# Kernel tuning notes

Hardware: AMD Instinct MI355X
Metric: run time of the kernel (lower is better)

## Reference

```python
import jax, jax.numpy as jnp
import numpy as np

LAGS = 2
LATENT = 64          # latent_size; number of tiny per-dim MLPs
HID = 64             # hidden_dim of each MLP2
SLOPE = 0.2          # LeakyReLU negative slope
IN_DIM = LAGS * LATENT + 1  # 129: flattened lags + current value of dim i


def setup_inputs() -> dict:
    key = jax.random.key(0)
    k0, k1, k2, k3, k4 = jax.random.split(key, 5)
    B, LEN = 32, 512
    x = jax.random.normal(k0, (B, LEN + LAGS, LATENT), jnp.float32)
    # Stacked per-latent MLP2 params (num_layers=1):
    #   Linear(IN_DIM -> HID) + LeakyReLU(0.2) + Linear(HID -> 1)
    s1 = float(1.0 / np.sqrt(IN_DIM))
    s2 = float(1.0 / np.sqrt(HID))
    W1 = jax.random.uniform(k1, (LATENT, HID, IN_DIM), jnp.float32, -s1, s1)
    b1 = jax.random.uniform(k2, (LATENT, HID), jnp.float32, -s1, s1)
    W2 = jax.random.uniform(k3, (LATENT, HID), jnp.float32, -s2, s2)
    b2 = jax.random.uniform(k4, (LATENT,), jnp.float32, -s2, s2)
    return {"x": x, "W1": W1, "b1": b1, "W2": W2, "b2": b2}


def reference(x, W1, b1, W2, b2):
    B, T, xd = x.shape
    length = T - LAGS
    N = B * length
    # torch unfold(dim=1, size=LAGS+1, step=1).transpose(2,3) -> [B, length, LAGS+1, xd]
    idx = jnp.arange(length)[:, None] + jnp.arange(LAGS + 1)[None, :]
    win = x[:, idx]                                   # [B, length, LAGS+1, xd]
    lagsx = win[:, :, :-1].reshape(N, LAGS * xd)      # [N, LAGS*xd]
    xt = win[:, :, -1].reshape(N, xd)                 # [N, xd] current values per latent dim
    # gs[i] input = concat(lagsx, xt[:, i:i+1]); batch all latent dims at once.
    W1_lags = W1[:, :, :-1]                           # [L, H, LAGS*xd]
    w1_t = W1[:, :, -1]                               # [L, H] weight on the appended x_t column
    pre = (jnp.einsum('nd,lhd->nlh', lagsx, W1_lags)
           + xt[:, :, None] * w1_t[None]
           + b1[None])                                # [N, L, H]
    act = jnp.where(pre >= 0, pre, SLOPE * pre)       # LeakyReLU(0.2)
    residuals = jnp.einsum('nlh,lh->nl', act, W2) + b2[None]   # [N, L]
    # Analytic last column of the per-sample Jacobian (d residual_i / d x_t_i):
    dact = jnp.where(pre >= 0, 1.0, SLOPE)
    J_last = jnp.einsum('lh,nlh,lh->nl', W2, dact, w1_t)       # [N, L]
    logabsdet = jnp.sum(jnp.log(jnp.abs(J_last)), axis=-1)     # [N]
    return residuals.reshape(B, length, xd), logabsdet.reshape(B, length)
```

## Files before the change

### kernel.cpp

```cpp
#include <hip/hip_runtime.h>
#include <math.h>

#define SLOPE  0.2f
#define NB     32
#define LEN    512
#define LATENT 64
#define HID    64
#define IN_DIM 129
#define TROWS  514
#define NTOT   (NB * LEN)

typedef __attribute__((ext_vector_type(8)))  short bf16x8;
typedef __attribute__((ext_vector_type(16))) float f32x16;
typedef __attribute__((ext_vector_type(4)))  float f32x4;

struct alignas(8) US4 { unsigned short x, y, z, w; };

__device__ inline void bsplit(float v, unsigned short& hi, unsigned short& lo) {
    unsigned int u  = __builtin_bit_cast(unsigned int, v);
    unsigned int hb = (u + 0x7fffu + ((u >> 16) & 1u)) >> 16;
    hi = (unsigned short)hb;
    float fh = __builtin_bit_cast(float, hb << 16);
    float r  = v - fh;
    unsigned int u2 = __builtin_bit_cast(unsigned int, r);
    lo = (unsigned short)((u2 + 0x7fffu + ((u2 >> 16) & 1u)) >> 16);
}

__global__ __launch_bounds__(256)
void conv_w1(const float* __restrict__ W1g, unsigned short* __restrict__ W1f,
             float* __restrict__ W1t, float* __restrict__ out_lad) {
    const int idx = blockIdx.x * 256 + threadIdx.x;
    if (idx < NTOT) out_lad[idx] = 0.f;
    const int row  = idx >> 4;
    const int o    = idx & 15;
    const int ks   = o >> 1, hi32 = o & 1;
    const int l    = row >> 6, h = row & 63;
    const int i    = h >> 5,  r32 = h & 31;
    const int lane = hi32 * 32 + r32;
    const float* src = W1g + (size_t)row * IN_DIM + o * 8;
    unsigned short hh[8], ll[8];
    #pragma unroll
    for (int e = 0; e < 8; ++e) bsplit(src[e], hh[e], ll[e]);
    const size_t base = (size_t)l * 16384 + (size_t)i * 8192 + (size_t)ks * 1024
                      + (size_t)lane * 8;
    *reinterpret_cast<US4*>(W1f + base)       = US4{hh[0], hh[1], hh[2], hh[3]};
    *reinterpret_cast<US4*>(W1f + base + 4)   = US4{hh[4], hh[5], hh[6], hh[7]};
    *reinterpret_cast<US4*>(W1f + base + 512) = US4{ll[0], ll[1], ll[2], ll[3]};
    *reinterpret_cast<US4*>(W1f + base + 516) = US4{ll[4], ll[5], ll[6], ll[7]};
    if (o == 15) W1t[row] = src[8];
}

__global__ __launch_bounds__(512, 2)
void fused_mfma(const float* __restrict__ xg,
                const float* __restrict__ b1g, const float* __restrict__ W2g,
                const float* __restrict__ b2g,
                const unsigned short* __restrict__ W1f,
                const float* __restrict__ W1t,
                float* __restrict__ out_res, float* __restrict__ out_lad)
{
    __shared__ unsigned short sXh[66][72];
    __shared__ unsigned short sXl[66][72];
    __shared__ float sXt[66][8];
    __shared__ float sJ[64][8];

    const int tid  = threadIdx.x;
    const int by   = blockIdx.x & 7;
    const int pt   = blockIdx.x >> 3;
    const int wn   = tid >> 6;
    const int lane = tid & 63;
    const int r32  = lane & 31;
    const int hi32 = lane >> 5;
    const int l    = by * 8 + wn;

    const unsigned short* A0 = W1f + (size_t)l * 16384 + (size_t)lane * 8;
    bf16x8 awh[2][8], awl[2][8];
    #pragma unroll
    for (int i = 0; i < 2; ++i)
        #pragma unroll
        for (int ks = 0; ks < 8; ++ks) {
            const unsigned short* p = A0 + i * 8192 + ks * 1024;
            awh[i][ks] = *reinterpret_cast<const bf16x8*>(p);
            awl[i][ks] = *reinterpret_cast<const bf16x8*>(p + 512);
        }

    #pragma unroll 1
    for (int s = 0; s < 8; ++s) {
        const size_t xrow0 = (size_t)pt * TROWS + s * 64;

        for (int i = tid; i < 66 * 16; i += 512) {
            const int row = i >> 4, c4 = (i & 15) << 2;
            const float4 v = *reinterpret_cast<const float4*>(
                xg + (xrow0 + row) * LATENT + c4);
            unsigned short h0,h1,h2,h3, l0,l1,l2,l3;
            bsplit(v.x, h0, l0); bsplit(v.y, h1, l1);
            bsplit(v.z, h2, l2); bsplit(v.w, h3, l3);
            *reinterpret_cast<US4*>(&sXh[row][c4]) = US4{h0, h1, h2, h3};
            *reinterpret_cast<US4*>(&sXl[row][c4]) = US4{l0, l1, l2, l3};
        }
        for (int i = tid; i < 66 * 8; i += 512) {
            const int row = i >> 3, w = i & 7;
            sXt[row][w] = xg[(xrow0 + row) * LATENT + by * 8 + w];
        }
        __syncthreads();

        f32x16 acc[2][2];
        #pragma unroll
        for (int i = 0; i < 2; ++i)
            #pragma unroll
            for (int g = 0; g < 4; ++g) {
                const f32x4 b14 = *reinterpret_cast<const f32x4*>(
                    b1g + l * HID + i * 32 + hi32 * 4 + g * 8);
                #pragma unroll
                for (int m = 0; m < 4; ++m) {
                    acc[i][0][g * 4 + m] = b14[m];
                    acc[i][1][g * 4 + m] = b14[m];
                }
            }

        #pragma unroll
        for (int ks = 0; ks < 8; ++ks) {
            const int lag = ks >> 2;
            const int cc  = (ks & 3) * 16 + hi32 * 8;
            bf16x8 bxh[2], bxl[2];
            #pragma unroll
            for (int j = 0; j < 2; ++j) {
                const int rr = j * 32 + r32 + lag;
                bxh[j] = *reinterpret_cast<const bf16x8*>(&sXh[rr][cc]);
                bxl[j] = *reinterpret_cast<const bf16x8*>(&sXl[rr][cc]);
            }
            #pragma unroll
            for (int i = 0; i < 2; ++i)
                #pragma unroll
                for (int j = 0; j < 2; ++j) {
                    acc[i][j] = __builtin_amdgcn_mfma_f32_32x32x16_bf16(awh[i][ks], bxh[j], acc[i][j], 0, 0, 0);
                    acc[i][j] = __builtin_amdgcn_mfma_f32_32x32x16_bf16(awh[i][ks], bxl[j], acc[i][j], 0, 0, 0);
                    acc[i][j] = __builtin_amdgcn_mfma_f32_32x32x16_bf16(awl[i][ks], bxh[j], acc[i][j], 0, 0, 0);
                }
        }

        const float xt0 = sXt[r32 + 2][wn];
        const float xt1 = sXt[32 + r32 + 2][wn];
        float res0 = 0.f, res1 = 0.f, jp0 = 0.f, jp1 = 0.f, jc = 0.f;

        #pragma unroll
        for (int i = 0; i < 2; ++i)
            #pragma unroll
            for (int g = 0; g < 4; ++g) {
                const int h0 = l * HID + i * 32 + hi32 * 4 + g * 8;
                const f32x4 wt = *reinterpret_cast<const f32x4*>(W1t + h0);
                const f32x4 w2 = *reinterpret_cast<const f32x4*>(W2g + h0);
                #pragma unroll
                for (int m = 0; m < 4; ++m) {
                    const float c0 = w2[m] * wt[m];
                    jc += c0;
                    const int r = g * 4 + m;
                    const float pre0 = fmaf(xt0, wt[m], acc[i][0][r]);
                    const float pre1 = fmaf(xt1, wt[m], acc[i][1][r]);
                    res0 += w2[m] * fmaxf(pre0, SLOPE * pre0);
                    res1 += w2[m] * fmaxf(pre1, SLOPE * pre1);
                    jp0 += (pre0 >= 0.f) ? c0 : 0.f;
                    jp1 += (pre1 >= 0.f) ? c0 : 0.f;
                }
            }

        res0 += __shfl_xor(res0, 32);
        res1 += __shfl_xor(res1, 32);
        jp0  += __shfl_xor(jp0, 32);
        jp1  += __shfl_xor(jp1, 32);
        jc   += __shfl_xor(jc, 32);
        const float jac0 = SLOPE * jc + (1.f - SLOPE) * jp0;
        const float jac1 = SLOPE * jc + (1.f - SLOPE) * jp1;

        const size_t nbase = (size_t)pt * LEN + s * 64;
        if (hi32 == 0) {
            const float b2v = b2g[l];
            const size_t n0 = nbase + r32;
            out_res[n0 * LATENT + l]        = res0 + b2v;
            out_res[(n0 + 32) * LATENT + l] = res1 + b2v;
            sJ[r32][wn]      = jac0;
            sJ[r32 + 32][wn] = jac1;
        }
        __syncthreads();
        if (tid < 64) {
            const float p = sJ[tid][0] * sJ[tid][1] * sJ[tid][2] * sJ[tid][3]
                          * sJ[tid][4] * sJ[tid][5] * sJ[tid][6] * sJ[tid][7];
            atomicAdd(&out_lad[nbase + tid], logf(fabsf(p)));
        }
        __syncthreads();
    }
}

extern "C" void kernel_launch(void* const* d_in, const int* in_sizes, int n_in,
                              void* d_out, int out_size, void* d_ws, size_t ws_size,
                              hipStream_t stream) {
    const float* xg  = (const float*)d_in[0];
    const float* W1g = (const float*)d_in[1];
    const float* b1g = (const float*)d_in[2];
    const float* W2g = (const float*)d_in[3];
    const float* b2g = (const float*)d_in[4];

    float* out_res = (float*)d_out;
    float* out_lad = out_res + (size_t)NTOT * LATENT;

    float*          W1t = (float*)d_ws;
    unsigned short* W1f = (unsigned short*)(W1t + 4096);

    conv_w1<<<256, 256, 0, stream>>>(W1g, W1f, W1t, out_lad);

    dim3 grid(256);
    fused_mfma<<<grid, 512, 0, stream>>>(xg, b1g, W2g, b2g, W1f, W1t,
                                         out_res, out_lad);
}
```

Baseline: 149.4 us.

## Split time loop across twice the blocks, stream W1 fragments, stage residual stores

```diff
diff --git a/kernel.cpp b/kernel.cpp
--- a/kernel.cpp
+++ b/kernel.cpp
@@ -62,10 +62,13 @@
     __shared__ unsigned short sXl[66][72];
     __shared__ float sXt[66][8];
     __shared__ float sJ[64][8];
+    __shared__ float sR[64][8];
 
     const int tid  = threadIdx.x;
     const int by   = blockIdx.x & 7;
-    const int pt   = blockIdx.x >> 3;
+    const int ht   = blockIdx.x >> 3;
+    const int pt   = ht >> 1;
+    const int s0   = (ht & 1) * 4;
     const int wn   = tid >> 6;
     const int lane = tid & 63;
     const int r32  = lane & 31;
@@ -73,18 +76,9 @@
     const int l    = by * 8 + wn;
 
     const unsigned short* A0 = W1f + (size_t)l * 16384 + (size_t)lane * 8;
-    bf16x8 awh[2][8], awl[2][8];
-    #pragma unroll
-    for (int i = 0; i < 2; ++i)
-        #pragma unroll
-        for (int ks = 0; ks < 8; ++ks) {
-            const unsigned short* p = A0 + i * 8192 + ks * 1024;
-            awh[i][ks] = *reinterpret_cast<const bf16x8*>(p);
-            awl[i][ks] = *reinterpret_cast<const bf16x8*>(p + 512);
-        }
 
     #pragma unroll 1
-    for (int s = 0; s < 8; ++s) {
+    for (int s = s0; s < s0 + 4; ++s) {
         const size_t xrow0 = (size_t)pt * TROWS + s * 64;
 
         for (int i = tid; i < 66 * 16; i += 512) {
@@ -121,7 +115,13 @@
         for (int ks = 0; ks < 8; ++ks) {
             const int lag = ks >> 2;
             const int cc  = (ks & 3) * 16 + hi32 * 8;
-            bf16x8 bxh[2], bxl[2];
+            const unsigned short* p0 = A0 + ks * 1024;
+            bf16x8 awh[2], awl[2], bxh[2], bxl[2];
+            #pragma unroll
+            for (int i = 0; i < 2; ++i) {
+                awh[i] = *reinterpret_cast<const bf16x8*>(p0 + i * 8192);
+                awl[i] = *reinterpret_cast<const bf16x8*>(p0 + i * 8192 + 512);
+            }
             #pragma unroll
             for (int j = 0; j < 2; ++j) {
                 const int rr = j * 32 + r32 + lag;
@@ -132,9 +132,9 @@
             for (int i = 0; i < 2; ++i)
                 #pragma unroll
                 for (int j = 0; j < 2; ++j) {
-                    acc[i][j] = __builtin_amdgcn_mfma_f32_32x32x16_bf16(awh[i][ks], bxh[j], acc[i][j], 0, 0, 0);
-                    acc[i][j] = __builtin_amdgcn_mfma_f32_32x32x16_bf16(awh[i][ks], bxl[j], acc[i][j], 0, 0, 0);
-                    acc[i][j] = __builtin_amdgcn_mfma_f32_32x32x16_bf16(awl[i][ks], bxh[j], acc[i][j], 0, 0, 0);
+                    acc[i][j] = __builtin_amdgcn_mfma_f32_32x32x16_bf16(awh[i], bxh[j], acc[i][j], 0, 0, 0);
+                    acc[i][j] = __builtin_amdgcn_mfma_f32_32x32x16_bf16(awh[i], bxl[j], acc[i][j], 0, 0, 0);
+                    acc[i][j] = __builtin_amdgcn_mfma_f32_32x32x16_bf16(awl[i], bxh[j], acc[i][j], 0, 0, 0);
                 }
         }
 
@@ -168,23 +168,26 @@
         jp0  += __shfl_xor(jp0, 32);
         jp1  += __shfl_xor(jp1, 32);
         jc   += __shfl_xor(jc, 32);
-        const float jac0 = SLOPE * jc + (1.f - SLOPE) * jp0;
-        const float jac1 = SLOPE * jc + (1.f - SLOPE) * jp1;
-
-        const size_t nbase = (size_t)pt * LEN + s * 64;
+
         if (hi32 == 0) {
             const float b2v = b2g[l];
-            const size_t n0 = nbase + r32;
-            out_res[n0 * LATENT + l]        = res0 + b2v;
-            out_res[(n0 + 32) * LATENT + l] = res1 + b2v;
-            sJ[r32][wn]      = jac0;
-            sJ[r32 + 32][wn] = jac1;
+            sR[r32][wn]      = res0 + b2v;
+            sR[r32 + 32][wn] = res1 + b2v;
+            sJ[r32][wn]      = SLOPE * jc + (1.f - SLOPE) * jp0;
+            sJ[r32 + 32][wn] = SLOPE * jc + (1.f - SLOPE) * jp1;
         }
         __syncthreads();
-        if (tid < 64) {
-            const float p = sJ[tid][0] * sJ[tid][1] * sJ[tid][2] * sJ[tid][3]
-                          * sJ[tid][4] * sJ[tid][5] * sJ[tid][6] * sJ[tid][7];
-            atomicAdd(&out_lad[nbase + tid], logf(fabsf(p)));
+
+        const size_t nbase = (size_t)pt * LEN + s * 64;
+        if (tid < 128) {
+            const int n = tid >> 1, part = (tid & 1) * 4;
+            *reinterpret_cast<f32x4*>(out_res + (nbase + n) * LATENT + by * 8 + part) =
+                *reinterpret_cast<const f32x4*>(&sR[n][part]);
+        } else if (tid >= 448) {
+            const int n = tid - 448;
+            const float p = sJ[n][0] * sJ[n][1] * sJ[n][2] * sJ[n][3]
+                          * sJ[n][4] * sJ[n][5] * sJ[n][6] * sJ[n][7];
+            atomicAdd(&out_lad[nbase + n], logf(fabsf(p)));
         }
         __syncthreads();
     }
@@ -207,7 +210,7 @@
 
     conv_w1<<<256, 256, 0, stream>>>(W1g, W1f, W1t, out_lad);
 
-    dim3 grid(256);
+    dim3 grid(512);
     fused_mfma<<<grid, 512, 0, stream>>>(xg, b1g, W2g, b2g, W1f, W1t,
                                          out_res, out_lad);
 }
```

Measured after the change: 157.3 us. 5.3% more time.

## Split latent dims across more blocks, remap grid per XCD, hoist epilogue weights

Applied to the files above, without the earlier changes.

```diff
diff --git a/kernel.cpp b/kernel.cpp
--- a/kernel.cpp
+++ b/kernel.cpp
@@ -50,7 +50,7 @@
     if (o == 15) W1t[row] = src[8];
 }
 
-__global__ __launch_bounds__(512, 2)
+__global__ __launch_bounds__(256, 2)
 void fused_mfma(const float* __restrict__ xg,
                 const float* __restrict__ b1g, const float* __restrict__ W2g,
                 const float* __restrict__ b2g,
@@ -60,17 +60,19 @@
 {
     __shared__ unsigned short sXh[66][72];
     __shared__ unsigned short sXl[66][72];
-    __shared__ float sXt[66][8];
-    __shared__ float sJ[64][8];
+    __shared__ float sXt[66][4];
+    __shared__ float sJ[64][4];
 
     const int tid  = threadIdx.x;
-    const int by   = blockIdx.x & 7;
-    const int pt   = blockIdx.x >> 3;
+    const int xcd  = blockIdx.x & 7;
+    const int k    = blockIdx.x >> 3;
+    const int pt   = xcd * 4 + (k & 3);
+    const int quad = k >> 2;
     const int wn   = tid >> 6;
     const int lane = tid & 63;
     const int r32  = lane & 31;
     const int hi32 = lane >> 5;
-    const int l    = by * 8 + wn;
+    const int l    = quad * 4 + wn;
 
     const unsigned short* A0 = W1f + (size_t)l * 16384 + (size_t)lane * 8;
     bf16x8 awh[2][8], awl[2][8];
@@ -83,11 +85,23 @@
             awl[i][ks] = *reinterpret_cast<const bf16x8*>(p + 512);
         }
 
+    float w1t[2][4][4], w2c[2][4][4], b1c[2][4][4];
+    #pragma unroll
+    for (int i = 0; i < 2; ++i)
+        #pragma unroll
+        for (int g = 0; g < 4; ++g) {
+            const int h0 = l * HID + i * 32 + hi32 * 4 + g * 8;
+            *reinterpret_cast<f32x4*>(w1t[i][g]) = *reinterpret_cast<const f32x4*>(W1t + h0);
+            *reinterpret_cast<f32x4*>(w2c[i][g]) = *reinterpret_cast<const f32x4*>(W2g + h0);
+            *reinterpret_cast<f32x4*>(b1c[i][g]) = *reinterpret_cast<const f32x4*>(b1g + h0);
+        }
+    const float b2v = b2g[l];
+
     #pragma unroll 1
     for (int s = 0; s < 8; ++s) {
         const size_t xrow0 = (size_t)pt * TROWS + s * 64;
 
-        for (int i = tid; i < 66 * 16; i += 512) {
+        for (int i = tid; i < 66 * 16; i += 256) {
             const int row = i >> 4, c4 = (i & 15) << 2;
             const float4 v = *reinterpret_cast<const float4*>(
                 xg + (xrow0 + row) * LATENT + c4);
@@ -97,9 +111,9 @@
             *reinterpret_cast<US4*>(&sXh[row][c4]) = US4{h0, h1, h2, h3};
             *reinterpret_cast<US4*>(&sXl[row][c4]) = US4{l0, l1, l2, l3};
         }
-        for (int i = tid; i < 66 * 8; i += 512) {
-            const int row = i >> 3, w = i & 7;
-            sXt[row][w] = xg[(xrow0 + row) * LATENT + by * 8 + w];
+        for (int i = tid; i < 66 * 4; i += 256) {
+            const int row = i >> 2, w = i & 3;
+            sXt[row][w] = xg[(xrow0 + row) * LATENT + quad * 4 + w];
         }
         __syncthreads();
 
@@ -107,15 +121,12 @@
         #pragma unroll
         for (int i = 0; i < 2; ++i)
             #pragma unroll
-            for (int g = 0; g < 4; ++g) {
-                const f32x4 b14 = *reinterpret_cast<const f32x4*>(
-                    b1g + l * HID + i * 32 + hi32 * 4 + g * 8);
+            for (int g = 0; g < 4; ++g)
                 #pragma unroll
                 for (int m = 0; m < 4; ++m) {
-                    acc[i][0][g * 4 + m] = b14[m];
-                    acc[i][1][g * 4 + m] = b14[m];
+                    acc[i][0][g * 4 + m] = b1c[i][g][m];
+                    acc[i][1][g * 4 + m] = b1c[i][g][m];
                 }
-            }
 
         #pragma unroll
         for (int ks = 0; ks < 8; ++ks) {
@@ -145,45 +156,37 @@
         #pragma unroll
         for (int i = 0; i < 2; ++i)
             #pragma unroll
-            for (int g = 0; g < 4; ++g) {
-                const int h0 = l * HID + i * 32 + hi32 * 4 + g * 8;
-                const f32x4 wt = *reinterpret_cast<const f32x4*>(W1t + h0);
-                const f32x4 w2 = *reinterpret_cast<const f32x4*>(W2g + h0);
+            for (int g = 0; g < 4; ++g)
                 #pragma unroll
                 for (int m = 0; m < 4; ++m) {
-                    const float c0 = w2[m] * wt[m];
+                    const float c0 = w2c[i][g][m] * w1t[i][g][m];
                     jc += c0;
                     const int r = g * 4 + m;
-                    const float pre0 = fmaf(xt0, wt[m], acc[i][0][r]);
-                    const float pre1 = fmaf(xt1, wt[m], acc[i][1][r]);
-                    res0 += w2[m] * fmaxf(pre0, SLOPE * pre0);
-                    res1 += w2[m] * fmaxf(pre1, SLOPE * pre1);
+                    const float pre0 = fmaf(xt0, w1t[i][g][m], acc[i][0][r]);
+                    const float pre1 = fmaf(xt1, w1t[i][g][m], acc[i][1][r]);
+                    res0 += w2c[i][g][m] * fmaxf(pre0, SLOPE * pre0);
+                    res1 += w2c[i][g][m] * fmaxf(pre1, SLOPE * pre1);
                     jp0 += (pre0 >= 0.f) ? c0 : 0.f;
                     jp1 += (pre1 >= 0.f) ? c0 : 0.f;
                 }
-            }
 
         res0 += __shfl_xor(res0, 32);
         res1 += __shfl_xor(res1, 32);
         jp0  += __shfl_xor(jp0, 32);
         jp1  += __shfl_xor(jp1, 32);
         jc   += __shfl_xor(jc, 32);
-        const float jac0 = SLOPE * jc + (1.f - SLOPE) * jp0;
-        const float jac1 = SLOPE * jc + (1.f - SLOPE) * jp1;
 
         const size_t nbase = (size_t)pt * LEN + s * 64;
         if (hi32 == 0) {
-            const float b2v = b2g[l];
             const size_t n0 = nbase + r32;
             out_res[n0 * LATENT + l]        = res0 + b2v;
             out_res[(n0 + 32) * LATENT + l] = res1 + b2v;
-            sJ[r32][wn]      = jac0;
-            sJ[r32 + 32][wn] = jac1;
+            sJ[r32][wn]      = SLOPE * jc + (1.f - SLOPE) * jp0;
+            sJ[r32 + 32][wn] = SLOPE * jc + (1.f - SLOPE) * jp1;
         }
         __syncthreads();
         if (tid < 64) {
-            const float p = sJ[tid][0] * sJ[tid][1] * sJ[tid][2] * sJ[tid][3]
-                          * sJ[tid][4] * sJ[tid][5] * sJ[tid][6] * sJ[tid][7];
+            const float p = sJ[tid][0] * sJ[tid][1] * sJ[tid][2] * sJ[tid][3];
             atomicAdd(&out_lad[nbase + tid], logf(fabsf(p)));
         }
         __syncthreads();
@@ -207,7 +210,7 @@
 
     conv_w1<<<256, 256, 0, stream>>>(W1g, W1f, W1t, out_lad);
 
-    dim3 grid(256);
-    fused_mfma<<<grid, 512, 0, stream>>>(xg, b1g, W2g, b2g, W1f, W1t,
+    dim3 grid(512);
+    fused_mfma<<<grid, 256, 0, stream>>>(xg, b1g, W2g, b2g, W1f, W1t,
                                          out_res, out_lad);
 }
```

After: 151.7 us. No clear change (+1.5%).
